# Kernel optimization log

Hardware: AMD Instinct MI355X
Metric: run time of the kernel (lower is better)

## Reference

```python
import jax, jax.numpy as jnp
import numpy as np
from jax import lax

EPS = 1e-5

def ste_sign(x):
    # forward-only module: plain sign is fine
    return jnp.sign(x)

def conv2d(x, w, pad):
    # x: NCHW, w: OIHW, stride 1
    return lax.conv_general_dilated(x, w, window_strides=(1, 1),
                                    padding=[(pad, pad), (pad, pad)],
                                    dimension_numbers=('NCHW', 'OIHW', 'NCHW'))

def maxpool2(x):
    # 2x2 max pool, stride 2, VALID (floor) -- matches nn.MaxPool2d(2,2)
    return lax.reduce_window(x, -jnp.inf, lax.max, (1, 1, 2, 2), (1, 1, 2, 2), 'VALID')

def batchnorm(x, gamma, beta):
    # training-mode BN: batch statistics over (N,H,W), biased variance
    mean = jnp.mean(x, axis=(0, 2, 3), keepdims=True)
    var = jnp.var(x, axis=(0, 2, 3), keepdims=True)
    xn = (x - mean) * lax.rsqrt(var + EPS)
    return xn * gamma[None, :, None, None] + beta[None, :, None, None]

def setup_inputs() -> dict:
    key = jax.random.key(0)
    ks = jax.random.split(key, 8)
    def he(k, shape):
        n = shape[2] * shape[3] * shape[0]
        return jax.random.normal(k, shape, jnp.float32) * np.sqrt(2.0 / n)
    x = jax.random.normal(ks[0], (4096, 1, 28, 28), jnp.float32)
    w0 = he(ks[1], (32, 1, 3, 3))
    w1 = he(ks[2], (32, 32, 3, 3))
    w2 = he(ks[3], (32, 32, 3, 3))
    g0 = jnp.ones((32,), jnp.float32); b0 = jnp.zeros((32,), jnp.float32)
    g1 = jnp.ones((32,), jnp.float32); b1 = jnp.zeros((32,), jnp.float32)
    g2 = jnp.ones((32,), jnp.float32); b2 = jnp.zeros((32,), jnp.float32)
    fw = jax.random.normal(ks[4], (10, 288), jnp.float32) * 0.01
    fb = jnp.zeros((10,), jnp.float32)
    return {"x": x, "w0": w0, "g0": g0, "b0": b0, "w1": w1, "g1": g1, "b1": b1,
            "w2": w2, "g2": g2, "b2": b2, "fw": fw, "fb": fb}

def reference(x, w0, g0, b0, w1, g1, b1, w2, g2, b2, fw, fb):
    # block0: fp conv -> pool -> bn (no act)
    h = batchnorm(maxpool2(conv2d(x, w0, 1)), g0, b0)          # [B,32,14,14]
    # block1: binary(1w1a) conv -> pool -> bn + maxpool(shortcut)
    o = batchnorm(maxpool2(conv2d(ste_sign(h), ste_sign(w1), 1)), g1, b1)
    h = o + maxpool2(h)                                         # [B,32,7,7]
    # block2
    o = batchnorm(maxpool2(conv2d(ste_sign(h), ste_sign(w2), 1)), g2, b2)
    h = o + maxpool2(h)                                         # [B,32,3,3]
    h = h.reshape(h.shape[0], -1)                                # [B,288]
    return h @ fw.T + fb                                         # [B,10]
```

## Files before the change

kernel.cpp:

```cpp
#include <hip/hip_runtime.h>
#include <stdint.h>

#define BATCH 4096

typedef float v16f __attribute__((ext_vector_type(16)));
typedef short v8s  __attribute__((ext_vector_type(8)));

__device__ __forceinline__ int sgn8(float v) {
    return (v > 0.f) ? 1 : ((v < 0.f) ? -1 : 0);
}

__global__ __launch_bounds__(448) void k_conv0s(const float* __restrict__ x,
                                                const float* __restrict__ w0,
                                                const float* __restrict__ w1,
                                                const float* __restrict__ w2,
                                                uint16_t* __restrict__ w1f,
                                                uint16_t* __restrict__ w2f,
                                                double* __restrict__ part0) {
    __shared__ float xs[960];
    __shared__ float wl[288];
    __shared__ double rs[448], rq[448];
    int n = blockIdx.x, t = threadIdx.x;

    if (n < 72 && t < 256) {
        int i = n * 256 + t;
        int ii = (i < 9216) ? i : i - 9216;
        const float* w = (i < 9216) ? w1 : w2;
        uint16_t* o = (i < 9216) ? w1f : w2f;
        int j = ii & 7, nn = (ii >> 3) & 31, q2 = (ii >> 8) & 1, kh = (ii >> 9) & 1, tp = ii >> 10;
        int cin = kh * 16 + q2 * 8 + j;
        float v = w[(nn * 32 + cin) * 9 + tp];
        o[ii] = (v > 0.f) ? 0x3F80 : ((v < 0.f) ? 0xBF80 : 0);
    }

    for (int i = t; i < 960; i += 448) xs[i] = 0.f;
    for (int i = t; i < 288; i += 448) wl[i] = w0[i];
    __syncthreads();
    for (int i = t; i < 784; i += 448) {
        int y = i / 28, xx = i - y * 28;
        xs[(y + 1) * 32 + xx + 1] = x[n * 784 + i];
    }
    __syncthreads();
    int c = t & 31, py = t >> 5;
    float wreg[9];
    #pragma unroll
    for (int i = 0; i < 9; ++i) wreg[i] = wl[c * 9 + i];
    const float4* X4 = (const float4*)xs;
    float4 cur0 = X4[(2 * py + 0) * 8];
    float4 cur1 = X4[(2 * py + 1) * 8];
    float4 cur2 = X4[(2 * py + 2) * 8];
    float4 cur3 = X4[(2 * py + 3) * 8];
    double s = 0.0, q = 0.0;
    #pragma unroll
    for (int k = 0; k < 7; ++k) {
        float4 n0 = X4[(2 * py + 0) * 8 + k + 1];
        float4 n1 = X4[(2 * py + 1) * 8 + k + 1];
        float4 n2 = X4[(2 * py + 2) * 8 + k + 1];
        float4 n3 = X4[(2 * py + 3) * 8 + k + 1];
        float a[4][6];
        a[0][0] = cur0.x; a[0][1] = cur0.y; a[0][2] = cur0.z; a[0][3] = cur0.w; a[0][4] = n0.x; a[0][5] = n0.y;
        a[1][0] = cur1.x; a[1][1] = cur1.y; a[1][2] = cur1.z; a[1][3] = cur1.w; a[1][4] = n1.x; a[1][5] = n1.y;
        a[2][0] = cur2.x; a[2][1] = cur2.y; a[2][2] = cur2.z; a[2][3] = cur2.w; a[2][4] = n2.x; a[2][5] = n2.y;
        a[3][0] = cur3.x; a[3][1] = cur3.y; a[3][2] = cur3.z; a[3][3] = cur3.w; a[3][4] = n3.x; a[3][5] = n3.y;
        #pragma unroll
        for (int e = 0; e < 2; ++e) {
            int base = 2 * e;
            float s00 = 0.f, s01 = 0.f, s10 = 0.f, s11 = 0.f;
            #pragma unroll
            for (int ky = 0; ky < 3; ++ky)
            #pragma unroll
            for (int kx = 0; kx < 3; ++kx) {
                float w = wreg[ky * 3 + kx];
                s00 = fmaf(a[ky][base + kx], w, s00);
                s01 = fmaf(a[ky][base + kx + 1], w, s01);
                s10 = fmaf(a[ky + 1][base + kx], w, s10);
                s11 = fmaf(a[ky + 1][base + kx + 1], w, s11);
            }
            float m = fmaxf(fmaxf(s00, s01), fmaxf(s10, s11));
            double v = (double)m;
            s += v; q += v * v;
        }
        cur0 = n0; cur1 = n1; cur2 = n2; cur3 = n3;
    }
    rs[c * 14 + py] = s; rq[c * 14 + py] = q;
    __syncthreads();
    if (t < 32) {
        double S = 0.0, Q = 0.0;
        #pragma unroll
        for (int i = 0; i < 14; ++i) { S += rs[t * 14 + i]; Q += rq[t * 14 + i]; }
        part0[(size_t)t * 4096 + n] = S;
        part0[(size_t)32 * 4096 + (size_t)t * 4096 + n] = Q;
    }
}

__global__ __launch_bounds__(256) void k_finalize(const double* __restrict__ part, int G,
                                                  const float* __restrict__ g,
                                                  const float* __restrict__ b,
                                                  double inv_count, float* __restrict__ ss) {
    int c = blockIdx.x, t = threadIdx.x;
    double s = 0.0, q = 0.0;
    for (int i = t; i < G; i += 256) {
        s += part[(size_t)c * G + i];
        q += part[(size_t)32 * G + (size_t)c * G + i];
    }
    #pragma unroll
    for (int o = 32; o > 0; o >>= 1) { s += __shfl_down(s, o); q += __shfl_down(q, o); }
    __shared__ double rs[4], rq[4];
    int w = t >> 6, l = t & 63;
    if (l == 0) { rs[w] = s; rq[w] = q; }
    __syncthreads();
    if (t == 0) {
        s = rs[0] + rs[1] + rs[2] + rs[3];
        q = rq[0] + rq[1] + rq[2] + rq[3];
        double mean = s * inv_count;
        double var = q * inv_count - mean * mean;
        double sc = (double)g[c] / sqrt(var + 1e-5);
        ss[c] = (float)sc;
        ss[32 + c] = (float)((double)b[c] - mean * sc);
    }
}

__global__ __launch_bounds__(448) void k_bn0r(const float* __restrict__ x,
                                              const float* __restrict__ w0,
                                              const float* __restrict__ ss,
                                              uint32_t* __restrict__ s0b,
                                              float* __restrict__ hp0) {
    __shared__ float xs[960];
    __shared__ float wl[288];
    __shared__ float P[6468];
    int n = blockIdx.x, t = threadIdx.x;
    for (int i = t; i < 960; i += 448) xs[i] = 0.f;
    for (int i = t; i < 288; i += 448) wl[i] = w0[i];
    __syncthreads();
    for (int i = t; i < 784; i += 448) {
        int y = i / 28, xx = i - y * 28;
        xs[(y + 1) * 32 + xx + 1] = x[n * 784 + i];
    }
    __syncthreads();
    int c = t & 31, py = t >> 5;
    float wreg[9];
    #pragma unroll
    for (int i = 0; i < 9; ++i) wreg[i] = wl[c * 9 + i];
    float sc = ss[c], sh = ss[32 + c];
    const float4* X4 = (const float4*)xs;
    float4 cur0 = X4[(2 * py + 0) * 8];
    float4 cur1 = X4[(2 * py + 1) * 8];
    float4 cur2 = X4[(2 * py + 2) * 8];
    float4 cur3 = X4[(2 * py + 3) * 8];
    #pragma unroll
    for (int k = 0; k < 7; ++k) {
        float4 n0 = X4[(2 * py + 0) * 8 + k + 1];
        float4 n1 = X4[(2 * py + 1) * 8 + k + 1];
        float4 n2 = X4[(2 * py + 2) * 8 + k + 1];
        float4 n3 = X4[(2 * py + 3) * 8 + k + 1];
        float a[4][6];
        a[0][0] = cur0.x; a[0][1] = cur0.y; a[0][2] = cur0.z; a[0][3] = cur0.w; a[0][4] = n0.x; a[0][5] = n0.y;
        a[1][0] = cur1.x; a[1][1] = cur1.y; a[1][2] = cur1.z; a[1][3] = cur1.w; a[1][4] = n1.x; a[1][5] = n1.y;
        a[2][0] = cur2.x; a[2][1] = cur2.y; a[2][2] = cur2.z; a[2][3] = cur2.w; a[2][4] = n2.x; a[2][5] = n2.y;
        a[3][0] = cur3.x; a[3][1] = cur3.y; a[3][2] = cur3.z; a[3][3] = cur3.w; a[3][4] = n3.x; a[3][5] = n3.y;
        #pragma unroll
        for (int e = 0; e < 2; ++e) {
            int base = 2 * e;
            float s00 = 0.f, s01 = 0.f, s10 = 0.f, s11 = 0.f;
            #pragma unroll
            for (int ky = 0; ky < 3; ++ky)
            #pragma unroll
            for (int kx = 0; kx < 3; ++kx) {
                float w = wreg[ky * 3 + kx];
                s00 = fmaf(a[ky][base + kx], w, s00);
                s01 = fmaf(a[ky][base + kx + 1], w, s01);
                s10 = fmaf(a[ky + 1][base + kx], w, s10);
                s11 = fmaf(a[ky + 1][base + kx + 1], w, s11);
            }
            float m = fmaxf(fmaxf(s00, s01), fmaxf(s10, s11));
            P[(py * 14 + 2 * k + e) * 33 + c] = fmaf(sc, m, sh);
        }
        cur0 = n0; cur1 = n1; cur2 = n2; cur3 = n3;
    }
    __syncthreads();
    uint32_t* simg = s0b + (size_t)n * 4096;
    for (int i = t; i < 784; i += 448) {
        int pl = i >> 2, qd = i & 3;
        int iy = pl / 14, ix = pl - iy * 14;
        int yy = iy + 1, xx2 = ix + 1;
        int p = yy * 16 + xx2;
        int psw = (xx2 & 3) ^ (yy & 3);
        int g = qd ^ psw;
        const float* Pp = &P[pl * 33 + g * 8];
        uint32_t d[4];
        #pragma unroll
        for (int j = 0; j < 4; ++j) {
            float h0 = Pp[2 * j], h1 = Pp[2 * j + 1];
            uint32_t b0 = (h0 > 0.f) ? 0x3F80u : ((h0 < 0.f) ? 0xBF80u : 0u);
            uint32_t b1 = (h1 > 0.f) ? 0x3F80u : ((h1 < 0.f) ? 0xBF80u : 0u);
            d[j] = b0 | (b1 << 16);
        }
        uint4 v; v.x = d[0]; v.y = d[1]; v.z = d[2]; v.w = d[3];
        *(uint4*)(simg + p * 16 + qd * 4) = v;
    }
    if (t < 240) {
        int e = t >> 2, qd = t & 3;
        int yh, xh;
        if (e < 16)      { yh = 0;      xh = e; }
        else if (e < 32) { yh = 15;     xh = e - 16; }
        else if (e < 46) { yh = e - 31; xh = 0; }
        else             { yh = e - 45; xh = 15; }
        uint4 z; z.x = z.y = z.z = z.w = 0u;
        *(uint4*)(simg + (yh * 16 + xh) * 16 + qd * 4) = z;
    }
    if (t < 196) {
        int pw = t >> 2, oct = t & 3;
        int pyy = pw / 7, pxx = pw - pyy * 7;
        int b00 = ((2 * pyy) * 14 + 2 * pxx) * 33;
        int b01 = b00 + 33;
        int b10 = b00 + 14 * 33;
        int b11 = b10 + 33;
        float out[8];
        #pragma unroll
        for (int k = 0; k < 8; ++k) {
            int cc = oct * 8 + k;
            out[k] = fmaxf(fmaxf(P[b00 + cc], P[b01 + cc]),
                           fmaxf(P[b10 + cc], P[b11 + cc]));
        }
        float4* hd = (float4*)(hp0 + ((size_t)n * 49 + pw) * 32 + oct * 8);
        float4 h0; h0.x = out[0]; h0.y = out[1]; h0.z = out[2]; h0.w = out[3];
        float4 h1; h1.x = out[4]; h1.y = out[5]; h1.z = out[6]; h1.w = out[7];
        hd[0] = h0; hd[1] = h1;
    }
}

__global__ __launch_bounds__(256) void k_conv1m(const uint32_t* __restrict__ s0b,
                                                const uint16_t* __restrict__ w1f,
                                                float* __restrict__ p1,
                                                double* __restrict__ part1) {
    __shared__ uint32_t lds[8192];
    int t = threadIdx.x;
    int n0 = blockIdx.x * 2;
    const uint4* gp = (const uint4*)(s0b + (size_t)n0 * 4096);
    uint4* lp = (uint4*)lds;
    #pragma unroll
    for (int i = 0; i < 8; ++i) lp[t + i * 256] = gp[t + i * 256];
    int lane = t & 63, wv = t >> 6;
    int q = lane >> 5, ncol = lane & 31;
    v8s wfr[18];
    #pragma unroll
    for (int f = 0; f < 18; ++f)
        wfr[f] = *(const v8s*)(w1f + (f * 2 + q) * 256 + ncol * 8);
    __syncthreads();
    int img = wv >> 1, wh = wv & 1;
    int n = n0 + img;
    int ibase = img * 4096;
    int m = lane & 31;
    int quad = m & 3, pwl = m >> 2;
    int dy = quad >> 1, dx = quad & 1;
    double sAcc = 0.0, qAcc = 0.0;
    for (int tile = wh; tile < 7; tile += 2) {
        int pw = tile * 8 + pwl;
        int pwc = min(pw, 48);
        int py = pwc / 7, px = pwc - py * 7;
        int pbase = (2 * py + dy) * 16 + 2 * px + dx;
        v16f acc;
        #pragma unroll
        for (int i = 0; i < 16; ++i) acc[i] = 0.f;
        #pragma unroll
        for (int tp = 0; tp < 9; ++tp) {
            int p = pbase + (tp / 3) * 16 + (tp % 3);
            int psw = (p ^ (p >> 4)) & 3;
            #pragma unroll
            for (int kh = 0; kh < 2; ++kh) {
                int g = kh * 2 + q;
                int idx = ibase + p * 16 + ((g ^ psw) << 2);
                v8s a = *(const v8s*)&lds[idx];
                acc = __builtin_amdgcn_mfma_f32_32x32x16_bf16(a, wfr[tp * 2 + kh], acc, 0, 0, 0);
            }
        }
        #pragma unroll
        for (int g4 = 0; g4 < 4; ++g4) {
            float mx = fmaxf(fmaxf(acc[4 * g4], acc[4 * g4 + 1]),
                             fmaxf(acc[4 * g4 + 2], acc[4 * g4 + 3]));
            int pwo = tile * 8 + 2 * g4 + q;
            if (pwo < 49) {
                p1[((size_t)n * 49 + pwo) * 32 + ncol] = mx;
                double v = (double)mx;
                sAcc += v; qAcc += v * v;
            }
        }
    }
    __syncthreads();
    double* red = (double*)lds;
    red[(wv * 2 + q) * 32 + ncol] = sAcc;
    red[256 + (wv * 2 + q) * 32 + ncol] = qAcc;
    __syncthreads();
    if (t < 32) {
        double S = 0.0, Q = 0.0;
        #pragma unroll
        for (int i = 0; i < 8; ++i) { S += red[i * 32 + t]; Q += red[256 + i * 32 + t]; }
        part1[(size_t)t * 2048 + blockIdx.x] = S;
        part1[(size_t)32 * 2048 + (size_t)t * 2048 + blockIdx.x] = Q;
    }
}

__global__ __launch_bounds__(256) void k_bn1(const float* __restrict__ p1,
                                             const float* __restrict__ hp0,
                                             const float* __restrict__ ss,
                                             uint32_t* __restrict__ s1a,
                                             float* __restrict__ hp1) {
    __shared__ float H[1568];
    int n = blockIdx.x, t = threadIdx.x;
    const float* P = p1 + (size_t)n * 1568;
    const float* Hp = hp0 + (size_t)n * 1568;
    for (int i = t; i < 1568; i += 256) {
        int c = i & 31;
        H[i] = fmaf(ss[64 + c], P[i], ss[96 + c]) + Hp[i];
    }
    __syncthreads();
    uint32_t* sp = s1a + (size_t)n * 1024;
    #pragma unroll
    for (int ii = 0; ii < 4; ++ii) {
        int i = t + ii * 256;
        int p = i >> 4, r = i & 15;
        int y = p >> 3, xq = p & 7;
        uint32_t d = 0u;
        if (y >= 1 && xq >= 1) {
            int pix = (y - 1) * 7 + (xq - 1);
            int sub = r & 3;
            int g = (r >> 2) ^ (p & 3);
            int c0 = ((g << 2) | sub) * 2;
            float h0 = H[pix * 32 + c0];
            float h1 = H[pix * 32 + c0 + 1];
            uint32_t b0 = (h0 > 0.f) ? 0x3F80u : ((h0 < 0.f) ? 0xBF80u : 0u);
            uint32_t b1 = (h1 > 0.f) ? 0x3F80u : ((h1 < 0.f) ? 0xBF80u : 0u);
            d = b0 | (b1 << 16);
        }
        sp[i] = d;
    }
    for (int jj = t; jj < 288; jj += 256) {
        int c = jj / 9, pix = jj - c * 9;
        int r = pix / 3, qq = pix - r * 3;
        float a0 = H[((2 * r) * 7 + 2 * qq) * 32 + c];
        float a1 = H[((2 * r) * 7 + 2 * qq + 1) * 32 + c];
        float a2 = H[((2 * r + 1) * 7 + 2 * qq) * 32 + c];
        float a3 = H[((2 * r + 1) * 7 + 2 * qq + 1) * 32 + c];
        hp1[n * 288 + c * 9 + pix] = fmaxf(fmaxf(a0, a1), fmaxf(a2, a3));
    }
}

__global__ __launch_bounds__(256) void k_conv2m(const uint32_t* __restrict__ s1a,
                                                const uint16_t* __restrict__ w2f,
                                                float* __restrict__ p2,
                                                double* __restrict__ part2) {
    __shared__ uint32_t lds[8192];
    int t = threadIdx.x;
    int n0 = blockIdx.x * 8;
    const uint4* gp4 = (const uint4*)(s1a + (size_t)n0 * 1024);
    uint4* lp = (uint4*)lds;
    #pragma unroll
    for (int i = 0; i < 8; ++i) lp[t + i * 256] = gp4[t + i * 256];
    int lane = t & 63, wv = t >> 6;
    int q = lane >> 5, ncol = lane & 31;
    v8s wfr[18];
    #pragma unroll
    for (int f = 0; f < 18; ++f)
        wfr[f] = *(const v8s*)(w2f + (f * 2 + q) * 256 + ncol * 8);
    __syncthreads();
    int m = lane & 31;
    int quad = m & 3, pwl = m >> 2;
    int dy = quad >> 1, dx = quad & 1;
    double sAcc = 0.0, qAcc = 0.0;
    for (int tile = wv; tile < 9; tile += 4) {
        int pwg = tile * 8 + pwl;
        int img = pwg / 9, pwi = pwg - img * 9;
        int py = pwi / 3, px = pwi - py * 3;
        int pbase = (2 * py + dy) * 8 + 2 * px + dx;
        v16f acc;
        #pragma unroll
        for (int i = 0; i < 16; ++i) acc[i] = 0.f;
        #pragma unroll
        for (int tp = 0; tp < 9; ++tp) {
            int p = pbase + (tp / 3) * 8 + (tp % 3);
            int psw = p & 3;
            #pragma unroll
            for (int kh = 0; kh < 2; ++kh) {
                int g = kh * 2 + q;
                int idx = img * 1024 + p * 16 + ((g ^ psw) << 2);
                v8s a = *(const v8s*)&lds[idx];
                acc = __builtin_amdgcn_mfma_f32_32x32x16_bf16(a, wfr[tp * 2 + kh], acc, 0, 0, 0);
            }
        }
        #pragma unroll
        for (int g4 = 0; g4 < 4; ++g4) {
            float mx = fmaxf(fmaxf(acc[4 * g4], acc[4 * g4 + 1]),
                             fmaxf(acc[4 * g4 + 2], acc[4 * g4 + 3]));
            int pwo = tile * 8 + 2 * g4 + q;
            int oimg = pwo / 9, opwi = pwo - oimg * 9;
            p2[(size_t)(n0 + oimg) * 288 + ncol * 9 + opwi] = mx;
            double v = (double)mx;
            sAcc += v; qAcc += v * v;
        }
    }
    __syncthreads();
    double* red = (double*)lds;
    red[(wv * 2 + q) * 32 + ncol] = sAcc;
    red[256 + (wv * 2 + q) * 32 + ncol] = qAcc;
    __syncthreads();
    if (t < 32) {
        double S = 0.0, Q = 0.0;
        #pragma unroll
        for (int i = 0; i < 8; ++i) { S += red[i * 32 + t]; Q += red[256 + i * 32 + t]; }
        part2[(size_t)t * 512 + blockIdx.x] = S;
        part2[(size_t)32 * 512 + (size_t)t * 512 + blockIdx.x] = Q;
    }
}

__global__ __launch_bounds__(256) void k_fc(const float* __restrict__ p2,
                                            const float* __restrict__ hp1,
                                            const float* __restrict__ ss,
                                            const float* __restrict__ fw,
                                            const float* __restrict__ fb,
                                            float* __restrict__ outv) {
    int wv = threadIdx.x >> 6, l = threadIdx.x & 63;
    int n = blockIdx.x * 4 + wv;
    float acc[10];
    #pragma unroll
    for (int k = 0; k < 10; ++k) acc[k] = 0.f;
    #pragma unroll
    for (int i = 0; i < 5; ++i) {
        int j = l + 64 * i;
        if (j < 288) {
            int c = j / 9;
            float h = fmaf(ss[128 + c], p2[n * 288 + j], ss[160 + c]) + hp1[n * 288 + j];
            #pragma unroll
            for (int k = 0; k < 10; ++k)
                acc[k] = fmaf(h, fw[k * 288 + j], acc[k]);
        }
    }
    #pragma unroll
    for (int k = 0; k < 10; ++k) {
        float s = acc[k];
        #pragma unroll
        for (int o = 32; o > 0; o >>= 1) s += __shfl_down(s, o);
        if (l == 0) outv[n * 10 + k] = s + fb[k];
    }
}

extern "C" void kernel_launch(void* const* d_in, const int* in_sizes, int n_in,
                              void* d_out, int out_size, void* d_ws, size_t ws_size,
                              hipStream_t stream) {
    (void)in_sizes; (void)n_in; (void)out_size; (void)ws_size;
    const float* x  = (const float*)d_in[0];
    const float* w0 = (const float*)d_in[1];
    const float* g0 = (const float*)d_in[2];
    const float* b0 = (const float*)d_in[3];
    const float* w1 = (const float*)d_in[4];
    const float* g1 = (const float*)d_in[5];
    const float* b1 = (const float*)d_in[6];
    const float* w2 = (const float*)d_in[7];
    const float* g2 = (const float*)d_in[8];
    const float* b2 = (const float*)d_in[9];
    const float* fw = (const float*)d_in[10];
    const float* fb = (const float*)d_in[11];
    float* outv = (float*)d_out;
    char* ws = (char*)d_ws;

    float*     ss    = (float*)(ws + 1024);
    uint16_t*  w1f   = (uint16_t*)(ws + 2048);
    uint16_t*  w2f   = (uint16_t*)(ws + 38912);
    float*     p1    = (float*)(ws + 76800);
    float*     hp1   = (float*)(ws + 32582656);
    float*     p2    = (float*)(ws + 37301248);
    uint32_t*  s0b   = (uint32_t*)(ws + 42019840);
    uint32_t*  s1a   = (uint32_t*)(ws + 42019840);
    double*    part0 = (double*)(ws + 109128704);
    double*    part1 = (double*)(ws + 111225856);
    double*    part2 = (double*)(ws + 112274432);
    float*     hp0   = (float*)(ws + 128527360);

    k_conv0s<<<BATCH, 448, 0, stream>>>(x, w0, w1, w2, w1f, w2f, part0);
    k_finalize<<<32, 256, 0, stream>>>(part0, 4096, g0, b0, 1.0 / (BATCH * 196.0), ss);
    k_bn0r<<<BATCH, 448, 0, stream>>>(x, w0, ss, s0b, hp0);

    k_conv1m<<<BATCH / 2, 256, 0, stream>>>(s0b, w1f, p1, part1);
    k_finalize<<<32, 256, 0, stream>>>(part1, 2048, g1, b1, 1.0 / (BATCH * 49.0), ss + 64);
    k_bn1<<<BATCH, 256, 0, stream>>>(p1, hp0, ss, s1a, hp1);

    k_conv2m<<<BATCH / 8, 256, 0, stream>>>(s1a, w2f, p2, part2);
    k_finalize<<<32, 256, 0, stream>>>(part2, 512, g2, b2, 1.0 / (BATCH * 9.0), ss + 128);

    k_fc<<<BATCH / 4, 256, 0, stream>>>(p2, hp1, ss, fw, fb, outv);
}
```

Before: 211.4 us.

## Fuse BN1/residual/sign packing into conv2 kernel, dropping s1a buffer

The separate k_bn1 kernel is merged into the conv2 MFMA kernel. Each block now applies BN1 scale and shift plus the residual for its 8 images, with software-prefetched float4 loads. It writes the packed sign activations straight into LDS and also emits the pooled shortcut hp1. This removes one launch and the global write and reread of the s1a activation buffer. In exchange the BN work is serialized per image inside fewer blocks (512 instead of 4096), and LDS use and barrier count go up.

```diff
diff --git a/kernel.cpp b/kernel.cpp
--- a/kernel.cpp
+++ b/kernel.cpp
@@ -300,69 +300,97 @@
     }
 }
 
-__global__ __launch_bounds__(256) void k_bn1(const float* __restrict__ p1,
-                                             const float* __restrict__ hp0,
-                                             const float* __restrict__ ss,
-                                             uint32_t* __restrict__ s1a,
-                                             float* __restrict__ hp1) {
-    __shared__ float H[1568];
-    int n = blockIdx.x, t = threadIdx.x;
-    const float* P = p1 + (size_t)n * 1568;
-    const float* Hp = hp0 + (size_t)n * 1568;
-    for (int i = t; i < 1568; i += 256) {
-        int c = i & 31;
-        H[i] = fmaf(ss[64 + c], P[i], ss[96 + c]) + Hp[i];
-    }
-    __syncthreads();
-    uint32_t* sp = s1a + (size_t)n * 1024;
-    #pragma unroll
-    for (int ii = 0; ii < 4; ++ii) {
-        int i = t + ii * 256;
-        int p = i >> 4, r = i & 15;
-        int y = p >> 3, xq = p & 7;
-        uint32_t d = 0u;
-        if (y >= 1 && xq >= 1) {
-            int pix = (y - 1) * 7 + (xq - 1);
-            int sub = r & 3;
-            int g = (r >> 2) ^ (p & 3);
-            int c0 = ((g << 2) | sub) * 2;
-            float h0 = H[pix * 32 + c0];
-            float h1 = H[pix * 32 + c0 + 1];
-            uint32_t b0 = (h0 > 0.f) ? 0x3F80u : ((h0 < 0.f) ? 0xBF80u : 0u);
-            uint32_t b1 = (h1 > 0.f) ? 0x3F80u : ((h1 < 0.f) ? 0xBF80u : 0u);
-            d = b0 | (b1 << 16);
-        }
-        sp[i] = d;
-    }
-    for (int jj = t; jj < 288; jj += 256) {
-        int c = jj / 9, pix = jj - c * 9;
-        int r = pix / 3, qq = pix - r * 3;
-        float a0 = H[((2 * r) * 7 + 2 * qq) * 32 + c];
-        float a1 = H[((2 * r) * 7 + 2 * qq + 1) * 32 + c];
-        float a2 = H[((2 * r + 1) * 7 + 2 * qq) * 32 + c];
-        float a3 = H[((2 * r + 1) * 7 + 2 * qq + 1) * 32 + c];
-        hp1[n * 288 + c * 9 + pix] = fmaxf(fmaxf(a0, a1), fmaxf(a2, a3));
-    }
-}
-
-__global__ __launch_bounds__(256) void k_conv2m(const uint32_t* __restrict__ s1a,
-                                                const uint16_t* __restrict__ w2f,
-                                                float* __restrict__ p2,
-                                                double* __restrict__ part2) {
+__global__ __launch_bounds__(256) void k_bc2m(const float* __restrict__ p1,
+                                              const float* __restrict__ hp0,
+                                              const float* __restrict__ ss,
+                                              const uint16_t* __restrict__ w2f,
+                                              float* __restrict__ p2,
+                                              float* __restrict__ hp1,
+                                              double* __restrict__ part2) {
     __shared__ uint32_t lds[8192];
+    __shared__ float Htmp[1568];
     int t = threadIdx.x;
     int n0 = blockIdx.x * 8;
-    const uint4* gp4 = (const uint4*)(s1a + (size_t)n0 * 1024);
-    uint4* lp = (uint4*)lds;
-    #pragma unroll
-    for (int i = 0; i < 8; ++i) lp[t + i * 256] = gp4[t + i * 256];
     int lane = t & 63, wv = t >> 6;
     int q = lane >> 5, ncol = lane & 31;
     v8s wfr[18];
     #pragma unroll
     for (int f = 0; f < 18; ++f)
         wfr[f] = *(const v8s*)(w2f + (f * 2 + q) * 256 + ncol * 8);
-    __syncthreads();
+
+    int cbase = (t & 7) * 4;
+    float sc4[4], sh4[4];
+    #pragma unroll
+    for (int j = 0; j < 4; ++j) { sc4[j] = ss[64 + cbase + j]; sh4[j] = ss[96 + cbase + j]; }
+
+    float4 pa, pb, ha, hb;
+    {
+        const float4* P4 = (const float4*)(p1 + (size_t)n0 * 1568);
+        const float4* H4 = (const float4*)(hp0 + (size_t)n0 * 1568);
+        pa = P4[t]; ha = H4[t];
+        if (t < 136) { pb = P4[256 + t]; hb = H4[256 + t]; }
+    }
+
+    float4* Ht4 = (float4*)Htmp;
+    for (int img = 0; img < 8; ++img) {
+        float4 npa, npb, nha, nhb;
+        if (img < 7) {
+            const float4* P4 = (const float4*)(p1 + (size_t)(n0 + img + 1) * 1568);
+            const float4* H4 = (const float4*)(hp0 + (size_t)(n0 + img + 1) * 1568);
+            npa = P4[t]; nha = H4[t];
+            if (t < 136) { npb = P4[256 + t]; nhb = H4[256 + t]; }
+        }
+        if (img) __syncthreads();
+        {
+            float4 hv;
+            hv.x = fmaf(sc4[0], pa.x, sh4[0]) + ha.x;
+            hv.y = fmaf(sc4[1], pa.y, sh4[1]) + ha.y;
+            hv.z = fmaf(sc4[2], pa.z, sh4[2]) + ha.z;
+            hv.w = fmaf(sc4[3], pa.w, sh4[3]) + ha.w;
+            Ht4[t] = hv;
+            if (t < 136) {
+                float4 hw;
+                hw.x = fmaf(sc4[0], pb.x, sh4[0]) + hb.x;
+                hw.y = fmaf(sc4[1], pb.y, sh4[1]) + hb.y;
+                hw.z = fmaf(sc4[2], pb.z, sh4[2]) + hb.z;
+                hw.w = fmaf(sc4[3], pb.w, sh4[3]) + hb.w;
+                Ht4[256 + t] = hw;
+            }
+        }
+        __syncthreads();
+        uint32_t* ap = &lds[img * 1024];
+        #pragma unroll
+        for (int ii = 0; ii < 4; ++ii) {
+            int i = t + ii * 256;
+            int pp = i >> 4, r = i & 15;
+            int y = pp >> 3, xq = pp & 7;
+            uint32_t d = 0u;
+            if (y >= 1 && xq >= 1) {
+                int pix = (y - 1) * 7 + (xq - 1);
+                int sub = r & 3;
+                int g = (r >> 2) ^ (pp & 3);
+                int c0 = ((g << 2) | sub) * 2;
+                float h0 = Htmp[pix * 32 + c0];
+                float h1 = Htmp[pix * 32 + c0 + 1];
+                uint32_t b0 = (h0 > 0.f) ? 0x3F80u : ((h0 < 0.f) ? 0xBF80u : 0u);
+                uint32_t b1 = (h1 > 0.f) ? 0x3F80u : ((h1 < 0.f) ? 0xBF80u : 0u);
+                d = b0 | (b1 << 16);
+            }
+            ap[i] = d;
+        }
+        for (int jj = t; jj < 288; jj += 256) {
+            int c = jj / 9, pix = jj - c * 9;
+            int r = pix / 3, qq = pix - r * 3;
+            float a0 = Htmp[((2 * r) * 7 + 2 * qq) * 32 + c];
+            float a1 = Htmp[((2 * r) * 7 + 2 * qq + 1) * 32 + c];
+            float a2 = Htmp[((2 * r + 1) * 7 + 2 * qq) * 32 + c];
+            float a3 = Htmp[((2 * r + 1) * 7 + 2 * qq + 1) * 32 + c];
+            hp1[(size_t)(n0 + img) * 288 + c * 9 + pix] = fmaxf(fmaxf(a0, a1), fmaxf(a2, a3));
+        }
+        pa = npa; pb = npb; ha = nha; hb = nhb;
+    }
+    __syncthreads();
+
     int m = lane & 31;
     int quad = m & 3, pwl = m >> 2;
     int dy = quad >> 1, dx = quad & 1;
@@ -469,7 +497,6 @@
     float*     hp1   = (float*)(ws + 32582656);
     float*     p2    = (float*)(ws + 37301248);
     uint32_t*  s0b   = (uint32_t*)(ws + 42019840);
-    uint32_t*  s1a   = (uint32_t*)(ws + 42019840);
     double*    part0 = (double*)(ws + 109128704);
     double*    part1 = (double*)(ws + 111225856);
     double*    part2 = (double*)(ws + 112274432);
@@ -481,9 +508,8 @@
 
     k_conv1m<<<BATCH / 2, 256, 0, stream>>>(s0b, w1f, p1, part1);
     k_finalize<<<32, 256, 0, stream>>>(part1, 2048, g1, b1, 1.0 / (BATCH * 49.0), ss + 64);
-    k_bn1<<<BATCH, 256, 0, stream>>>(p1, hp0, ss, s1a, hp1);
-
-    k_conv2m<<<BATCH / 8, 256, 0, stream>>>(s1a, w2f, p2, part2);
+
+    k_bc2m<<<BATCH / 8, 256, 0, stream>>>(p1, hp0, ss, w2f, p2, hp1, part2);
     k_finalize<<<32, 256, 0, stream>>>(part2, 512, g2, b2, 1.0 / (BATCH * 9.0), ss + 128);
 
     k_fc<<<BATCH / 4, 256, 0, stream>>>(p2, hp1, ss, fw, fb, outv);
```

New measurement: 203.8 us. 1.04x faster.
